# Kernel optimization log

Measured on AMD Instinct MI355X. Metric: run time of the kernel, lower is better.

## Reference

```python
import jax, jax.numpy as jnp
import numpy as np

E = 2048
H = 16
D = E // H  # head_dim = 128
S_SLOTS = 8
EPS = 1e-5


def _linear_params(key, fan_in, fan_out):
    kw, kb = jax.random.split(key)
    lim = 1.0 / np.sqrt(fan_in)
    W = jax.random.uniform(kw, (fan_out, fan_in), jnp.float32, -lim, lim)
    b = jax.random.uniform(kb, (fan_out,), jnp.float32, -lim, lim)
    return W, b


def setup_inputs() -> dict:
    key = jax.random.key(0)
    ks = jax.random.split(key, 10)
    x = jax.random.normal(ks[0], (2, 2048, E), jnp.float32)
    thought_slots = jax.random.normal(ks[1], (S_SLOTS, E), jnp.float32)
    Wq, bq = _linear_params(ks[2], E, E)
    Wk, bk = _linear_params(ks[3], E, E)
    Wv, bv = _linear_params(ks[4], E, E)
    Wtq, btq = _linear_params(ks[5], E, E)
    Wtk, btk = _linear_params(ks[6], E, E)
    Wtv, btv = _linear_params(ks[7], E, E)
    Wo, bo = _linear_params(ks[8], E, E)
    gamma = jnp.ones((E,), jnp.float32)
    beta = jnp.zeros((E,), jnp.float32)
    return dict(x=x, thought_slots=thought_slots, Wq=Wq, bq=bq, Wk=Wk, bk=bk,
                Wv=Wv, bv=bv, Wtq=Wtq, btq=btq, Wtk=Wtk, btk=btk,
                Wtv=Wtv, btv=btv, Wo=Wo, bo=bo, gamma=gamma, beta=beta)


def _heads(t, B):
    # [B, S, E] -> [B, H, S, D]
    return t.reshape(B, -1, H, D).transpose(0, 2, 1, 3)


def reference(x, thought_slots, Wq, bq, Wk, bk, Wv, bv,
              Wtq, btq, Wtk, btk, Wtv, btv, Wo, bo, gamma, beta):
    B, S, _ = x.shape
    scale = 1.0 / np.sqrt(D)

    # regular self-attention stream
    q = _heads(x @ Wq.T + bq, B)
    k = _heads(x @ Wk.T + bk, B)
    v = _heads(x @ Wv.T + bv, B)
    attn = jax.nn.softmax(jnp.einsum('bhqd,bhkd->bhqk', q, k) * scale, axis=-1)
    regular_out = jnp.einsum('bhqk,bhkd->bhqd', attn, v)

    # thought cross-attention stream (keys/values from learned slots)
    slots = jnp.broadcast_to(thought_slots, (B, S_SLOTS, thought_slots.shape[-1]))
    t_q = _heads(x @ Wtq.T + btq, B)
    t_k = _heads(slots @ Wtk.T + btk, B)
    t_v = _heads(slots @ Wtv.T + btv, B)
    t_attn = jax.nn.softmax(jnp.einsum('bhqd,bhkd->bhqk', t_q, t_k) * scale, axis=-1)
    thought_out = jnp.einsum('bhqk,bhkd->bhqd', t_attn, t_v)

    # merge heads, combine, layernorm, output projection
    combined = (regular_out + thought_out).transpose(0, 2, 1, 3).reshape(B, S, E)
    mu = jnp.mean(combined, axis=-1, keepdims=True)
    var = jnp.var(combined, axis=-1, keepdims=True)
    normed = (combined - mu) * jax.lax.rsqrt(var + EPS) * gamma + beta
    return normed @ Wo.T + bo
```

## Files before the change

kernel.cpp:

```cpp
#include <hip/hip_runtime.h>
#include <hip/hip_bf16.h>
#include <stdint.h>

typedef __bf16 bf16;
typedef __bf16 bf16x8 __attribute__((ext_vector_type(8)));
typedef __bf16 bf16x4 __attribute__((ext_vector_type(4)));
typedef float f32x4 __attribute__((ext_vector_type(4)));

#define E_DIM 2048
#define HEADS 16
#define HD 128
#define SEQ 2048
#define BATCH 2
#define NTOK 4096
#define NSLOT 8

#define QSCALE (0.08838834764831845f * 1.4426950408889634f)

__device__ __forceinline__ void gload_lds16(const void* g, void* lds) {
  __builtin_amdgcn_global_load_lds(
      (const __attribute__((address_space(1))) uint32_t*)g,
      (__attribute__((address_space(3))) uint32_t*)lds, 16, 0, 0);
}

__global__ __launch_bounds__(256) void cvt_f32_bf16_kernel(
    const float* __restrict__ src, bf16* __restrict__ dst, int n8)
{
  for (int i = blockIdx.x * 256 + threadIdx.x; i < n8; i += gridDim.x * 256) {
    const f32x4 a = *(const f32x4*)(src + i * 8);
    const f32x4 b = *(const f32x4*)(src + i * 8 + 4);
    bf16x8 o;
#pragma unroll
    for (int j = 0; j < 4; j++) { o[j] = (bf16)a[j]; o[4 + j] = (bf16)b[j]; }
    *(bf16x8*)(dst + i * 8) = o;
  }
}

struct ProjArgs {
  const bf16* W[4];
  const float* bias[4];
  void* out[4];
  int mode[4];
  float scale[4];
};

__global__ __launch_bounds__(512, 2) void gemm256_kernel(
    const bf16* __restrict__ A, ProjArgs pa, int nbm, int nbn)
{
  __shared__ bf16 As[2][256 * 64];
  __shared__ bf16 Bs[2][256 * 64];

  const int nwg = gridDim.x;
  const int qch = nwg >> 3;
  const int wg = (blockIdx.x & 7) * qch + (blockIdx.x >> 3);
  const int bm = wg % nbm;
  const int rest = wg / nbm;
  const int bn = rest % nbn;
  const int z = rest / nbn;

  const bf16* __restrict__ W = pa.W[z];
  const float* __restrict__ bias = pa.bias[z];
  void* __restrict__ out = pa.out[z];
  const int mode = pa.mode[z];
  const float scale = pa.scale[z];

  const int tid = threadIdx.x;
  const int lane = tid & 63;
  const int w = tid >> 6;
  const int wr = w >> 2;
  const int wc = w & 3;
  const int g = lane >> 4, c = lane & 15;

  const int rsub = lane >> 3;
  const int csub = ((lane & 7) ^ rsub) * 8;

  const int arow0 = wr * 128 + wc * 32;
  const int hb = wc >> 1, gj = (wr << 1) | (wc & 1);
  const int brow0 = hb * 128 + gj * 32;
  const bf16* Asrc = A + (size_t)(bm * 256 + arow0 + rsub) * 2048 + csub;
  const bf16* Bsrc = W + (size_t)(bn * 256 + brow0 + rsub) * 2048 + csub;

  auto stage = [&](int t, int buf) {
    const int k0 = t * 64;
    char* Adst = (char*)(&As[buf][0]) + arow0 * 128;
    char* Bdst = (char*)(&Bs[buf][0]) + brow0 * 128;
#pragma unroll
    for (int i = 0; i < 4; i++) {
      gload_lds16(Asrc + (size_t)(i * 8) * 2048 + k0, Adst + i * 1024);
      gload_lds16(Bsrc + (size_t)(i * 8) * 2048 + k0, Bdst + i * 1024);
    }
  };

  f32x4 acc[8][4] = {};

  stage(0, 0);
  __syncthreads();
  int cur = 0;

  const int NT = 2048 / 64;
  for (int t = 0; t < NT; t++) {
    if (t + 1 < NT) stage(t + 1, cur ^ 1);
#pragma unroll
    for (int kk = 0; kk < 2; kk++) {
      bf16x8 bfr[4], af[8];
#pragma unroll
      for (int n = 0; n < 4; n++) {
        const int row = wc * 64 + n * 16 + c;
        bfr[n] = *(const bf16x8*)((const char*)(&Bs[cur][0]) + row * 128 +
                                  (((kk * 4 + g) ^ (c & 7)) * 16));
      }
#pragma unroll
      for (int mi = 0; mi < 8; mi++) {
        const int row = wr * 128 + mi * 16 + c;
        af[mi] = *(const bf16x8*)((const char*)(&As[cur][0]) + row * 128 +
                                  (((kk * 4 + g) ^ (c & 7)) * 16));
      }
      __builtin_amdgcn_s_setprio(1);
#pragma unroll
      for (int mi = 0; mi < 8; mi++)
#pragma unroll
        for (int n = 0; n < 4; n++)
          acc[mi][n] = __builtin_amdgcn_mfma_f32_16x16x32_bf16(af[mi], bfr[n], acc[mi][n], 0, 0, 0);
      __builtin_amdgcn_s_setprio(0);
    }
    __syncthreads();
    cur ^= 1;
  }

#pragma unroll
  for (int mi = 0; mi < 8; mi++) {
#pragma unroll
    for (int n = 0; n < 4; n++) {
      const int col = bn * 256 + wc * 64 + n * 16 + c;
      const float bv = bias[col];
#pragma unroll
      for (int j = 0; j < 4; j++) {
        const int row = bm * 256 + wr * 128 + mi * 16 + g * 4 + j;
        const float v = (acc[mi][n][j] + bv) * scale;
        if (mode == 0) {
          ((float*)out)[(size_t)row * E_DIM + col] = v;
        } else {
          const int b = row >> 11, s = row & 2047;
          const int h = col >> 7, d = col & 127;
          size_t idx;
          if (mode == 1) idx = (((size_t)(b * HEADS + h)) * SEQ + s) * HD + d;
          else           idx = (((size_t)(b * HEADS + h)) * HD + d) * SEQ + s;
          ((bf16*)out)[idx] = (bf16)v;
        }
      }
    }
  }
}

__global__ __launch_bounds__(256) void gemm_nt_kernel(
    const bf16* __restrict__ A, ProjArgs pa, int M, int N, int K)
{
  __shared__ bf16 As[2][128 * 32];
  __shared__ bf16 Bs[2][128 * 32];

  const int z = blockIdx.z;
  const bf16* __restrict__ W = pa.W[z];
  const float* __restrict__ bias = pa.bias[z];
  void* __restrict__ out = pa.out[z];
  const int mode = pa.mode[z];
  const float scale = pa.scale[z];

  const int tid = threadIdx.x;
  const int lane = tid & 63;
  const int w = tid >> 6;
  const int wr = w >> 1, wc = w & 1;
  const int g = lane >> 4, c = lane & 15;
  const int bm = blockIdx.x, bn = blockIdx.y;

  f32x4 acc[4][4] = {};

  const int srow = lane >> 2;
  const int scol = (lane & 3) * 8;
  const bf16* Ab = A + (size_t)(bm * 128 + srow) * K + scol;
  const bf16* Wb = W + (size_t)(bn * 128 + srow) * K + scol;

  auto stage = [&](int k0, int buf) {
#pragma unroll
    for (int i = 0; i < 2; ++i) {
      const int chunk = w * 2 + i;
      gload_lds16(Ab + (size_t)(chunk * 16) * K + k0, (char*)(&As[buf][0]) + chunk * 1024);
      gload_lds16(Wb + (size_t)(chunk * 16) * K + k0, (char*)(&Bs[buf][0]) + chunk * 1024);
    }
  };

  stage(0, 0);
  __syncthreads();
  int cur = 0;

  for (int k0 = 0; k0 < K; k0 += 32) {
    if (k0 + 32 < K) stage(k0 + 32, cur ^ 1);
    bf16x8 af[4], bfr[4];
#pragma unroll
    for (int m = 0; m < 4; m++)
      af[m] = *(const bf16x8*)(&As[cur][0] + (wr * 64 + m * 16 + c) * 32 + g * 8);
#pragma unroll
    for (int n = 0; n < 4; n++)
      bfr[n] = *(const bf16x8*)(&Bs[cur][0] + (wc * 64 + n * 16 + c) * 32 + g * 8);
#pragma unroll
    for (int m = 0; m < 4; m++)
#pragma unroll
      for (int n = 0; n < 4; n++)
        acc[m][n] = __builtin_amdgcn_mfma_f32_16x16x32_bf16(af[m], bfr[n], acc[m][n], 0, 0, 0);
    __syncthreads();
    cur ^= 1;
  }

#pragma unroll
  for (int m = 0; m < 4; m++) {
#pragma unroll
    for (int n = 0; n < 4; n++) {
      const int col = bn * 128 + wc * 64 + n * 16 + c;
      const float bv = bias[col];
#pragma unroll
      for (int j = 0; j < 4; j++) {
        const int row = bm * 128 + wr * 64 + m * 16 + g * 4 + j;
        const float v = (acc[m][n][j] + bv) * scale;
        if (mode == 0) {
          ((float*)out)[(size_t)row * N + col] = v;
        } else {
          const int b = row >> 11, s = row & 2047;
          const int h = col >> 7, d = col & 127;
          size_t idx;
          if (mode == 1) idx = (((size_t)(b * HEADS + h)) * SEQ + s) * HD + d;
          else           idx = (((size_t)(b * HEADS + h)) * HD + d) * SEQ + s;
          ((bf16*)out)[idx] = (bf16)v;
        }
      }
    }
  }
}

__global__ __launch_bounds__(256) void slots_proj_kernel(
    const float* __restrict__ slots,
    const float* __restrict__ Wk, const float* __restrict__ bk,
    const float* __restrict__ Wv, const float* __restrict__ bv,
    float* __restrict__ tk, float* __restrict__ tv)
{
  const int col = blockIdx.x * 256 + threadIdx.x;
  const int slot = blockIdx.y;
  const int mat = blockIdx.z;
  const float* W = mat ? Wv : Wk;
  const float* bias = mat ? bv : bk;
  float* out = mat ? tv : tk;
  const float* xr = slots + (size_t)slot * E_DIM;
  const float* wr = W + (size_t)col * E_DIM;
  float acc = 0.f;
  for (int k = 0; k < E_DIM; k += 4) {
    const f32x4 a = *(const f32x4*)(xr + k);
    const f32x4 b4 = *(const f32x4*)(wr + k);
#pragma unroll
    for (int i = 0; i < 4; i++) acc += a[i] * b4[i];
  }
  out[(size_t)slot * E_DIM + col] = acc + bias[col];
}

__global__ __launch_bounds__(256) void flash_attn_kernel(
    const bf16* __restrict__ Qg, const bf16* __restrict__ Kg,
    const bf16* __restrict__ Vtg, bf16* __restrict__ Og)
{
  __shared__ char Ks[2][64 * 256];
  __shared__ char Vs[2][128 * 128];
  __shared__ char Ps[4][4096];

  const int orig = blockIdx.x;
  const int logical = (orig & 7) * 64 + (orig >> 3);
  const int qt = logical & 15;
  const int bh = logical >> 4;

  const int tid = threadIdx.x;
  const int lane = tid & 63;
  const int w = tid >> 6;
  const int g = lane >> 4, c = lane & 15;
  const int b = bh >> 4, h = bh & 15;
  const int q0 = qt * 128 + w * 32;

  const bf16* Qb = Qg + ((size_t)bh * SEQ + q0) * HD;
  const bf16* Kb = Kg + (size_t)bh * SEQ * HD;
  const bf16* Vb = Vtg + (size_t)bh * HD * SEQ;
  char* Pw = Ps[w];

  auto stage = [&](int kv0, int buf) {
#pragma unroll
    for (int i = 0; i < 4; i++) {
      const int chunk = w * 4 + i;
      const int p = chunk * 1024 + lane * 16;
      {
        const int r = p >> 8;
        const int sl = ((p >> 4) & 15) ^ (r & 7);
        gload_lds16(Kb + (size_t)(kv0 + r) * HD + sl * 8, &Ks[buf][0] + chunk * 1024);
      }
      {
        const int r = p >> 7;
        const int sl = ((p >> 4) & 7) ^ (r & 7);
        gload_lds16(Vb + (size_t)r * SEQ + kv0 + sl * 8, &Vs[buf][0] + chunk * 1024);
      }
    }
  };

  bf16x8 qf[4][2];
#pragma unroll
  for (int kk = 0; kk < 4; kk++)
#pragma unroll
    for (int n = 0; n < 2; n++)
      qf[kk][n] = *(const bf16x8*)(Qb + (size_t)(n * 16 + c) * HD + kk * 32 + g * 8);

  stage(0, 0);
  __syncthreads();
  int cur = 0;

  f32x4 acc[2][8] = {};
  float mrun[2] = {-1e30f, -1e30f};
  float lsum[2] = {0.f, 0.f};

  for (int kv0 = 0; kv0 < SEQ; kv0 += 64) {
    if (kv0 + 64 < SEQ) stage(kv0 + 64, cur ^ 1);

    f32x4 st[4][2] = {};
#pragma unroll
    for (int kk = 0; kk < 4; kk++) {
      bf16x8 kf[4];
#pragma unroll
      for (int kfr = 0; kfr < 4; kfr++) {
        const int r = kfr * 16 + c;
        const int sl = (kk * 4 + g) ^ (r & 7);
        kf[kfr] = *(const bf16x8*)(&Ks[cur][0] + r * 256 + sl * 16);
      }
      __builtin_amdgcn_s_setprio(1);
#pragma unroll
      for (int kfr = 0; kfr < 4; kfr++)
#pragma unroll
        for (int n = 0; n < 2; n++)
          st[kfr][n] = __builtin_amdgcn_mfma_f32_16x16x32_bf16(kf[kfr], qf[kk][n], st[kfr][n], 0, 0, 0);
      __builtin_amdgcn_s_setprio(0);
    }

    float fsc[2];
    bool anyresc = false;
#pragma unroll
    for (int n = 0; n < 2; n++) {
      float mt[8];
#pragma unroll
      for (int kfr = 0; kfr < 4; kfr++) {
        mt[kfr * 2]     = fmaxf(st[kfr][n][0], st[kfr][n][1]);
        mt[kfr * 2 + 1] = fmaxf(st[kfr][n][2], st[kfr][n][3]);
      }
#pragma unroll
      for (int i = 0; i < 4; i++) mt[i] = fmaxf(mt[i], mt[i + 4]);
      mt[0] = fmaxf(mt[0], mt[2]); mt[1] = fmaxf(mt[1], mt[3]);
      float lm = fmaxf(mt[0], mt[1]);
      lm = fmaxf(lm, __shfl_xor(lm, 16));
      lm = fmaxf(lm, __shfl_xor(lm, 32));
      if (__any(lm > mrun[n] + 8.0f)) {
        const float mn = fmaxf(mrun[n], lm);
        fsc[n] = exp2f(mrun[n] - mn);
        mrun[n] = mn;
        anyresc = true;
      } else {
        fsc[n] = 1.0f;
      }
      float stt[8];
#pragma unroll
      for (int kfr = 0; kfr < 4; kfr++) {
        float p0 = exp2f(st[kfr][n][0] - mrun[n]);
        float p1 = exp2f(st[kfr][n][1] - mrun[n]);
        float p2 = exp2f(st[kfr][n][2] - mrun[n]);
        float p3 = exp2f(st[kfr][n][3] - mrun[n]);
        st[kfr][n][0] = p0; st[kfr][n][1] = p1; st[kfr][n][2] = p2; st[kfr][n][3] = p3;
        stt[kfr * 2] = p0 + p1; stt[kfr * 2 + 1] = p2 + p3;
      }
#pragma unroll
      for (int i = 0; i < 4; i++) stt[i] += stt[i + 4];
      stt[0] += stt[2]; stt[1] += stt[3];
      lsum[n] = lsum[n] * fsc[n] + (stt[0] + stt[1]);
    }

    if (anyresc) {
#pragma unroll
      for (int m = 0; m < 2; m++)
#pragma unroll
        for (int j = 0; j < 4; j++) {
          const float fj = __shfl(fsc[m], (lane & 48) | (g * 4 + j));
#pragma unroll
          for (int n = 0; n < 8; n++) acc[m][n][j] *= fj;
        }
    }

#pragma unroll
    for (int n = 0; n < 2; n++)
#pragma unroll
      for (int kfr = 0; kfr < 4; kfr++) {
        bf16x4 pk;
#pragma unroll
        for (int j = 0; j < 4; j++) pk[j] = (bf16)st[kfr][n][j];
        const int q = n * 16 + c;
        const int L = q * 128 + kfr * 32 + g * 8;
        *(bf16x4*)(Pw + (L ^ ((q & 7) << 4))) = pk;
      }

#pragma unroll
    for (int kk = 0; kk < 2; kk++) {
      bf16x8 pf[2];
#pragma unroll
      for (int m = 0; m < 2; m++) {
        const int q = m * 16 + c;
        const int L = q * 128 + kk * 64 + g * 16;
        pf[m] = *(const bf16x8*)(Pw + (L ^ ((q & 7) << 4)));
      }
      __builtin_amdgcn_s_setprio(1);
#pragma unroll
      for (int n = 0; n < 8; n++) {
        const int d = n * 16 + c;
        const int Lv = d * 128 + kk * 64 + g * 16;
        const bf16x8 vf = *(const bf16x8*)(&Vs[cur][0] + (Lv ^ ((d & 7) << 4)));
#pragma unroll
        for (int m = 0; m < 2; m++)
          acc[m][n] = __builtin_amdgcn_mfma_f32_16x16x32_bf16(pf[m], vf, acc[m][n], 0, 0, 0);
      }
      __builtin_amdgcn_s_setprio(0);
    }

    __syncthreads();
    cur ^= 1;
  }

  float lrun[2];
#pragma unroll
  for (int n = 0; n < 2; n++) {
    float t = lsum[n];
    t += __shfl_xor(t, 16);
    t += __shfl_xor(t, 32);
    lrun[n] = t;
  }
#pragma unroll
  for (int m = 0; m < 2; m++) {
#pragma unroll
    for (int j = 0; j < 4; j++) {
      const float lb = __shfl(lrun[m], (lane & 48) | (g * 4 + j));
      const float linv = 1.0f / lb;
      const int s = q0 + m * 16 + g * 4 + j;
#pragma unroll
      for (int n = 0; n < 8; n++) {
        const int e = h * HD + n * 16 + c;
        Og[((size_t)b * SEQ + s) * E_DIM + e] = (bf16)(acc[m][n][j] * linv);
      }
    }
  }
}

__global__ __launch_bounds__(256) void thought_ln_kernel(
    const bf16* __restrict__ TQ, const float* __restrict__ TK,
    const float* __restrict__ TV, const bf16* __restrict__ ATT,
    const float* __restrict__ gamma, const float* __restrict__ beta,
    bf16* __restrict__ Y)
{
  __shared__ float wsum[4], wsq[4];
  const int tid = threadIdx.x;
  const int lane = tid & 63;
  const int w = tid >> 6;
  const int tok = blockIdx.x;
  const int b = tok >> 11, s = tok & 2047;
  const int e0 = tid * 8;
  const int h = e0 >> 7;
  const int d0 = e0 & 127;

  const bf16x8 av = *(const bf16x8*)(ATT + (size_t)tok * E_DIM + e0);
  float v[8];
#pragma unroll
  for (int i = 0; i < 8; i++) v[i] = (float)av[i];

  const bf16x8 qv8 = *(const bf16x8*)(TQ + (((size_t)(b * HEADS + h)) * SEQ + s) * HD + d0);
  float qv[8];
#pragma unroll
  for (int i = 0; i < 8; i++) qv[i] = (float)qv8[i];

  float dts[NSLOT];
#pragma unroll
  for (int sl = 0; sl < NSLOT; sl++) {
    const float* tkr = TK + (size_t)sl * E_DIM + e0;
    const f32x4 k0 = *(const f32x4*)(tkr);
    const f32x4 k1 = *(const f32x4*)(tkr + 4);
    float dp = 0.f;
#pragma unroll
    for (int i = 0; i < 4; i++) dp += qv[i] * k0[i] + qv[4 + i] * k1[i];
    dp += __shfl_xor(dp, 1);
    dp += __shfl_xor(dp, 2);
    dp += __shfl_xor(dp, 4);
    dp += __shfl_xor(dp, 8);
    dts[sl] = dp;
  }
  float mx = dts[0];
#pragma unroll
  for (int sl = 1; sl < NSLOT; sl++) mx = fmaxf(mx, dts[sl]);
  float p[NSLOT], den = 0.f;
#pragma unroll
  for (int sl = 0; sl < NSLOT; sl++) { p[sl] = exp2f(dts[sl] - mx); den += p[sl]; }
  const float dinv = 1.0f / den;
#pragma unroll
  for (int sl = 0; sl < NSLOT; sl++) {
    const float pn = p[sl] * dinv;
    const float* tvr = TV + (size_t)sl * E_DIM + e0;
    const f32x4 v0 = *(const f32x4*)(tvr);
    const f32x4 v1 = *(const f32x4*)(tvr + 4);
#pragma unroll
    for (int i = 0; i < 4; i++) { v[i] += pn * v0[i]; v[4 + i] += pn * v1[i]; }
  }

  float sm = 0.f, sq = 0.f;
#pragma unroll
  for (int i = 0; i < 8; i++) { sm += v[i]; sq += v[i] * v[i]; }
#pragma unroll
  for (int d = 1; d < 64; d <<= 1) { sm += __shfl_xor(sm, d); sq += __shfl_xor(sq, d); }
  if (lane == 0) { wsum[w] = sm; wsq[w] = sq; }
  __syncthreads();
  const float ts = wsum[0] + wsum[1] + wsum[2] + wsum[3];
  const float tq2 = wsq[0] + wsq[1] + wsq[2] + wsq[3];
  const float mean = ts * (1.f / E_DIM);
  const float var = tq2 * (1.f / E_DIM) - mean * mean;
  const float rstd = rsqrtf(var + 1e-5f);
  const f32x4 g0 = *(const f32x4*)(gamma + e0);
  const f32x4 g1 = *(const f32x4*)(gamma + e0 + 4);
  const f32x4 b0 = *(const f32x4*)(beta + e0);
  const f32x4 b1 = *(const f32x4*)(beta + e0 + 4);
  bf16x8 outv;
#pragma unroll
  for (int i = 0; i < 4; i++) {
    outv[i]     = (bf16)((v[i]     - mean) * rstd * g0[i] + b0[i]);
    outv[4 + i] = (bf16)((v[4 + i] - mean) * rstd * g1[i] + b1[i]);
  }
  *(bf16x8*)(Y + (size_t)tok * E_DIM + e0) = outv;
}

extern "C" void kernel_launch(void* const* d_in, const int* in_sizes, int n_in,
                              void* d_out, int out_size, void* d_ws, size_t ws_size,
                              hipStream_t stream) {
  (void)in_sizes; (void)n_in; (void)out_size; (void)ws_size;
  const float* x     = (const float*)d_in[0];
  const float* slots = (const float*)d_in[1];
  const float* Wq  = (const float*)d_in[2];   const float* bq  = (const float*)d_in[3];
  const float* Wk  = (const float*)d_in[4];   const float* bk  = (const float*)d_in[5];
  const float* Wv  = (const float*)d_in[6];   const float* bv  = (const float*)d_in[7];
  const float* Wtq = (const float*)d_in[8];   const float* btq = (const float*)d_in[9];
  const float* Wtk = (const float*)d_in[10];  const float* btk = (const float*)d_in[11];
  const float* Wtv = (const float*)d_in[12];  const float* btv = (const float*)d_in[13];
  const float* Wo  = (const float*)d_in[14];  const float* bo  = (const float*)d_in[15];
  const float* gamma = (const float*)d_in[16];
  const float* beta  = (const float*)d_in[17];

  uint8_t* ws = (uint8_t*)d_ws;
  const size_t BUF  = (size_t)NTOK * E_DIM * sizeof(bf16);
  const size_t WBUF = (size_t)E_DIM * E_DIM * sizeof(bf16);
  bf16* xb   = (bf16*)(ws + 0 * BUF);
  bf16* qb   = (bf16*)(ws + 1 * BUF);
  bf16* kb   = (bf16*)(ws + 2 * BUF);
  bf16* vtb  = (bf16*)(ws + 3 * BUF);
  bf16* tqb  = (bf16*)(ws + 4 * BUF);
  bf16* attb = (bf16*)(ws + 5 * BUF);
  bf16* nrmb = qb;
  uint8_t* wp = ws + 6 * BUF;
  bf16* Wqb  = (bf16*)(wp + 0 * WBUF);
  bf16* Wkb  = (bf16*)(wp + 1 * WBUF);
  bf16* Wvb  = (bf16*)(wp + 2 * WBUF);
  bf16* Wtqb = (bf16*)(wp + 3 * WBUF);
  bf16* Wob  = (bf16*)(wp + 4 * WBUF);
  float* tkb = (float*)(wp + 5 * WBUF);
  float* tvb = (float*)(wp + 5 * WBUF + 128 * 1024);

  const int WN8 = E_DIM * E_DIM / 8;
  const int XN8 = NTOK * E_DIM / 8;
  cvt_f32_bf16_kernel<<<dim3(2048), 256, 0, stream>>>(x, xb, XN8);
  cvt_f32_bf16_kernel<<<dim3(1024), 256, 0, stream>>>(Wq, Wqb, WN8);
  cvt_f32_bf16_kernel<<<dim3(1024), 256, 0, stream>>>(Wk, Wkb, WN8);
  cvt_f32_bf16_kernel<<<dim3(1024), 256, 0, stream>>>(Wv, Wvb, WN8);
  cvt_f32_bf16_kernel<<<dim3(1024), 256, 0, stream>>>(Wtq, Wtqb, WN8);
  cvt_f32_bf16_kernel<<<dim3(1024), 256, 0, stream>>>(Wo, Wob, WN8);

  ProjArgs pa;
  pa.W[0] = Wqb;  pa.bias[0] = bq;  pa.out[0] = qb;  pa.mode[0] = 1; pa.scale[0] = QSCALE;
  pa.W[1] = Wkb;  pa.bias[1] = bk;  pa.out[1] = kb;  pa.mode[1] = 1; pa.scale[1] = 1.0f;
  pa.W[2] = Wvb;  pa.bias[2] = bv;  pa.out[2] = vtb; pa.mode[2] = 2; pa.scale[2] = 1.0f;
  pa.W[3] = Wtqb; pa.bias[3] = btq; pa.out[3] = tqb; pa.mode[3] = 1; pa.scale[3] = QSCALE;
  gemm256_kernel<<<dim3(16 * 8 * 4), 512, 0, stream>>>(xb, pa, 16, 8);

  slots_proj_kernel<<<dim3(E_DIM / 256, NSLOT, 2), 256, 0, stream>>>(
      slots, Wtk, btk, Wtv, btv, tkb, tvb);

  flash_attn_kernel<<<dim3((SEQ / 128) * BATCH * HEADS), 256, 0, stream>>>(
      qb, kb, vtb, attb);
  thought_ln_kernel<<<dim3(NTOK), 256, 0, stream>>>(
      tqb, tkb, tvb, attb, gamma, beta, nrmb);

  ProjArgs po;
  po.W[0] = Wob; po.bias[0] = bo; po.out[0] = d_out; po.mode[0] = 0; po.scale[0] = 1.0f;
  po.W[1] = po.W[2] = po.W[3] = Wob;
  po.bias[1] = po.bias[2] = po.bias[3] = bo;
  po.out[1] = po.out[2] = po.out[3] = d_out;
  po.mode[1] = po.mode[2] = po.mode[3] = 0;
  po.scale[1] = po.scale[2] = po.scale[3] = 1.0f;
  gemm_nt_kernel<<<dim3(NTOK / 128, E_DIM / 128, 1), 256, 0, stream>>>(
      nrmb, po, NTOK, E_DIM, E_DIM);
}
```

Measured before the change: 523.9 us.

## Rewrite flash attention with 32x32 MFMA, register-resident P, 512-thread blocks

The flash attention kernel switches from 16x16x32 to 32x32x16 bf16 MFMA tiles, so each wave owns 32 query rows with a single running max and sum per lane. The P matrix is now rearranged in registers with a cross-half lane shuffle instead of a per-wave LDS round trip, which removes the Ps shared buffer and its write/read traffic. Blocks grow to 512 threads covering 256 queries, so each staged K/V tile is shared by eight waves, and the K swizzle widens to 16. The cost is higher register pressure from the f32x16 accumulators and half as many blocks in the grid, which may lower occupancy.

```diff
diff --git a/kernel.cpp b/kernel.cpp
--- a/kernel.cpp
+++ b/kernel.cpp
@@ -6,6 +6,9 @@
 typedef __bf16 bf16x8 __attribute__((ext_vector_type(8)));
 typedef __bf16 bf16x4 __attribute__((ext_vector_type(4)));
 typedef float f32x4 __attribute__((ext_vector_type(4)));
+typedef float f32x16 __attribute__((ext_vector_type(16)));
+typedef uint32_t u32x2 __attribute__((ext_vector_type(2)));
+typedef uint32_t u32x4 __attribute__((ext_vector_type(4)));
 
 #define E_DIM 2048
 #define HEADS 16
@@ -259,197 +262,161 @@
   out[(size_t)slot * E_DIM + col] = acc + bias[col];
 }
 
-__global__ __launch_bounds__(256) void flash_attn_kernel(
+__global__ __launch_bounds__(512) void flash_attn_kernel(
     const bf16* __restrict__ Qg, const bf16* __restrict__ Kg,
     const bf16* __restrict__ Vtg, bf16* __restrict__ Og)
 {
   __shared__ char Ks[2][64 * 256];
   __shared__ char Vs[2][128 * 128];
-  __shared__ char Ps[4][4096];
 
   const int orig = blockIdx.x;
-  const int logical = (orig & 7) * 64 + (orig >> 3);
-  const int qt = logical & 15;
-  const int bh = logical >> 4;
+  const int logical = (orig & 7) * 32 + (orig >> 3);
+  const int qt = logical & 7;
+  const int bh = logical >> 3;
 
   const int tid = threadIdx.x;
   const int lane = tid & 63;
   const int w = tid >> 6;
-  const int g = lane >> 4, c = lane & 15;
+  const int q = lane & 31;
+  const int hi = lane >> 5;
   const int b = bh >> 4, h = bh & 15;
-  const int q0 = qt * 128 + w * 32;
+  const int q0 = qt * 256 + w * 32;
 
   const bf16* Qb = Qg + ((size_t)bh * SEQ + q0) * HD;
   const bf16* Kb = Kg + (size_t)bh * SEQ * HD;
   const bf16* Vb = Vtg + (size_t)bh * HD * SEQ;
-  char* Pw = Ps[w];
 
   auto stage = [&](int kv0, int buf) {
 #pragma unroll
-    for (int i = 0; i < 4; i++) {
-      const int chunk = w * 4 + i;
-      const int p = chunk * 1024 + lane * 16;
-      {
-        const int r = p >> 8;
-        const int sl = ((p >> 4) & 15) ^ (r & 7);
-        gload_lds16(Kb + (size_t)(kv0 + r) * HD + sl * 8, &Ks[buf][0] + chunk * 1024);
-      }
-      {
-        const int r = p >> 7;
-        const int sl = ((p >> 4) & 7) ^ (r & 7);
-        gload_lds16(Vb + (size_t)r * SEQ + kv0 + sl * 8, &Vs[buf][0] + chunk * 1024);
-      }
+    for (int i = 0; i < 2; i++) {
+      const int p = (tid + i * 512) * 16;
+      { const int r = p >> 8; const int s16 = (p >> 4) & 15;
+        gload_lds16(Kb + (size_t)(kv0 + r) * HD + (s16 ^ (r & 15)) * 8, &Ks[buf][0] + p); }
+      { const int r = p >> 7; const int s8 = (p >> 4) & 7;
+        gload_lds16(Vb + (size_t)r * SEQ + kv0 + (s8 ^ (r & 7)) * 8, &Vs[buf][0] + p); }
     }
   };
 
-  bf16x8 qf[4][2];
-#pragma unroll
-  for (int kk = 0; kk < 4; kk++)
-#pragma unroll
-    for (int n = 0; n < 2; n++)
-      qf[kk][n] = *(const bf16x8*)(Qb + (size_t)(n * 16 + c) * HD + kk * 32 + g * 8);
+  bf16x8 qf[8];
+#pragma unroll
+  for (int kc = 0; kc < 8; kc++)
+    qf[kc] = *(const bf16x8*)(Qb + (size_t)q * HD + kc * 16 + hi * 8);
 
   stage(0, 0);
   __syncthreads();
   int cur = 0;
 
-  f32x4 acc[2][8] = {};
-  float mrun[2] = {-1e30f, -1e30f};
-  float lsum[2] = {0.f, 0.f};
+  f32x16 o[4] = {};
+  float mrun = -1e30f, lsum = 0.f;
 
   for (int kv0 = 0; kv0 < SEQ; kv0 += 64) {
     if (kv0 + 64 < SEQ) stage(kv0 + 64, cur ^ 1);
 
-    f32x4 st[4][2] = {};
-#pragma unroll
-    for (int kk = 0; kk < 4; kk++) {
-      bf16x8 kf[4];
-#pragma unroll
-      for (int kfr = 0; kfr < 4; kfr++) {
-        const int r = kfr * 16 + c;
-        const int sl = (kk * 4 + g) ^ (r & 7);
-        kf[kfr] = *(const bf16x8*)(&Ks[cur][0] + r * 256 + sl * 16);
-      }
-      __builtin_amdgcn_s_setprio(1);
-#pragma unroll
-      for (int kfr = 0; kfr < 4; kfr++)
-#pragma unroll
-        for (int n = 0; n < 2; n++)
-          st[kfr][n] = __builtin_amdgcn_mfma_f32_16x16x32_bf16(kf[kfr], qf[kk][n], st[kfr][n], 0, 0, 0);
-      __builtin_amdgcn_s_setprio(0);
-    }
-
-    float fsc[2];
-    bool anyresc = false;
-#pragma unroll
-    for (int n = 0; n < 2; n++) {
-      float mt[8];
-#pragma unroll
-      for (int kfr = 0; kfr < 4; kfr++) {
-        mt[kfr * 2]     = fmaxf(st[kfr][n][0], st[kfr][n][1]);
-        mt[kfr * 2 + 1] = fmaxf(st[kfr][n][2], st[kfr][n][3]);
-      }
-#pragma unroll
-      for (int i = 0; i < 4; i++) mt[i] = fmaxf(mt[i], mt[i + 4]);
-      mt[0] = fmaxf(mt[0], mt[2]); mt[1] = fmaxf(mt[1], mt[3]);
-      float lm = fmaxf(mt[0], mt[1]);
-      lm = fmaxf(lm, __shfl_xor(lm, 16));
-      lm = fmaxf(lm, __shfl_xor(lm, 32));
-      if (__any(lm > mrun[n] + 8.0f)) {
-        const float mn = fmaxf(mrun[n], lm);
-        fsc[n] = exp2f(mrun[n] - mn);
-        mrun[n] = mn;
-        anyresc = true;
-      } else {
-        fsc[n] = 1.0f;
-      }
-      float stt[8];
-#pragma unroll
-      for (int kfr = 0; kfr < 4; kfr++) {
-        float p0 = exp2f(st[kfr][n][0] - mrun[n]);
-        float p1 = exp2f(st[kfr][n][1] - mrun[n]);
-        float p2 = exp2f(st[kfr][n][2] - mrun[n]);
-        float p3 = exp2f(st[kfr][n][3] - mrun[n]);
-        st[kfr][n][0] = p0; st[kfr][n][1] = p1; st[kfr][n][2] = p2; st[kfr][n][3] = p3;
-        stt[kfr * 2] = p0 + p1; stt[kfr * 2 + 1] = p2 + p3;
-      }
-#pragma unroll
-      for (int i = 0; i < 4; i++) stt[i] += stt[i + 4];
-      stt[0] += stt[2]; stt[1] += stt[3];
-      lsum[n] = lsum[n] * fsc[n] + (stt[0] + stt[1]);
-    }
-
-    if (anyresc) {
-#pragma unroll
-      for (int m = 0; m < 2; m++)
-#pragma unroll
-        for (int j = 0; j < 4; j++) {
-          const float fj = __shfl(fsc[m], (lane & 48) | (g * 4 + j));
-#pragma unroll
-          for (int n = 0; n < 8; n++) acc[m][n][j] *= fj;
+    f32x16 st[2] = {};
+    __builtin_amdgcn_s_setprio(1);
+#pragma unroll
+    for (int kc = 0; kc < 8; kc++) {
+#pragma unroll
+      for (int blk = 0; blk < 2; blk++) {
+        const int rt = blk * 32 + q;
+        const int sl = (2 * kc + hi) ^ (rt & 15);
+        const bf16x8 kf = *(const bf16x8*)(&Ks[cur][0] + rt * 256 + sl * 16);
+        st[blk] = __builtin_amdgcn_mfma_f32_32x32x16_bf16(kf, qf[kc], st[blk], 0, 0, 0);
+      }
+    }
+    __builtin_amdgcn_s_setprio(0);
+
+    float t[16];
+#pragma unroll
+    for (int i = 0; i < 16; i++) t[i] = fmaxf(st[0][i], st[1][i]);
+#pragma unroll
+    for (int s2 = 8; s2 > 0; s2 >>= 1)
+#pragma unroll
+      for (int i = 0; i < 8; i++) if (i < s2) t[i] = fmaxf(t[i], t[i + s2]);
+    float lm = t[0];
+    lm = fmaxf(lm, __shfl_xor(lm, 32));
+
+    float fsc = 1.0f;
+    if (__any(lm > mrun + 8.0f)) {
+      const float mn = fmaxf(mrun, lm);
+      fsc = exp2f(mrun - mn);
+      mrun = mn;
+#pragma unroll
+      for (int db = 0; db < 4; db++)
+#pragma unroll
+        for (int i = 0; i < 16; i++) o[db][i] *= fsc;
+    }
+
+    float ps0 = 0.f, ps1 = 0.f, ps2 = 0.f, ps3 = 0.f;
+#pragma unroll
+    for (int blk = 0; blk < 2; blk++)
+#pragma unroll
+      for (int i = 0; i < 16; i += 4) {
+        const float p0 = exp2f(st[blk][i]     - mrun);
+        const float p1 = exp2f(st[blk][i + 1] - mrun);
+        const float p2 = exp2f(st[blk][i + 2] - mrun);
+        const float p3 = exp2f(st[blk][i + 3] - mrun);
+        st[blk][i] = p0; st[blk][i + 1] = p1; st[blk][i + 2] = p2; st[blk][i + 3] = p3;
+        ps0 += p0; ps1 += p1; ps2 += p2; ps3 += p3;
+      }
+    lsum = lsum * fsc + ((ps0 + ps1) + (ps2 + ps3));
+
+    bf16x8 pb[2][2];
+#pragma unroll
+    for (int blk = 0; blk < 2; blk++)
+#pragma unroll
+      for (int c = 0; c < 2; c++) {
+        bf16x4 Lv, Hv;
+#pragma unroll
+        for (int i = 0; i < 4; i++) {
+          Lv[i] = (bf16)st[blk][8 * c + i];
+          Hv[i] = (bf16)st[blk][8 * c + 4 + i];
         }
-    }
-
-#pragma unroll
-    for (int n = 0; n < 2; n++)
-#pragma unroll
-      for (int kfr = 0; kfr < 4; kfr++) {
-        bf16x4 pk;
-#pragma unroll
-        for (int j = 0; j < 4; j++) pk[j] = (bf16)st[kfr][n][j];
-        const int q = n * 16 + c;
-        const int L = q * 128 + kfr * 32 + g * 8;
-        *(bf16x4*)(Pw + (L ^ ((q & 7) << 4))) = pk;
-      }
-
-#pragma unroll
-    for (int kk = 0; kk < 2; kk++) {
-      bf16x8 pf[2];
-#pragma unroll
-      for (int m = 0; m < 2; m++) {
-        const int q = m * 16 + c;
-        const int L = q * 128 + kk * 64 + g * 16;
-        pf[m] = *(const bf16x8*)(Pw + (L ^ ((q & 7) << 4)));
-      }
-      __builtin_amdgcn_s_setprio(1);
-#pragma unroll
-      for (int n = 0; n < 8; n++) {
-        const int d = n * 16 + c;
-        const int Lv = d * 128 + kk * 64 + g * 16;
-        const bf16x8 vf = *(const bf16x8*)(&Vs[cur][0] + (Lv ^ ((d & 7) << 4)));
-#pragma unroll
-        for (int m = 0; m < 2; m++)
-          acc[m][n] = __builtin_amdgcn_mfma_f32_16x16x32_bf16(pf[m], vf, acc[m][n], 0, 0, 0);
-      }
-      __builtin_amdgcn_s_setprio(0);
-    }
+        const u32x2 Lu = __builtin_bit_cast(u32x2, Lv);
+        const u32x2 Hu = __builtin_bit_cast(u32x2, Hv);
+        const uint32_t s0 = hi ? Lu.x : Hu.x;
+        const uint32_t s1 = hi ? Lu.y : Hu.y;
+        const uint32_t x0 = (uint32_t)__shfl_xor((int)s0, 32);
+        const uint32_t x1 = (uint32_t)__shfl_xor((int)s1, 32);
+        u32x4 bv;
+        bv.x = hi ? x0 : Lu.x;
+        bv.y = hi ? x1 : Lu.y;
+        bv.z = hi ? Hu.x : x0;
+        bv.w = hi ? Hu.y : x1;
+        pb[blk][c] = __builtin_bit_cast(bf16x8, bv);
+      }
+
+    __builtin_amdgcn_s_setprio(1);
+#pragma unroll
+    for (int db = 0; db < 4; db++) {
+      const int rt = db * 32 + q;
+#pragma unroll
+      for (int blk = 0; blk < 2; blk++)
+#pragma unroll
+        for (int c = 0; c < 2; c++) {
+          const int sl = (blk * 4 + c * 2 + hi) ^ (rt & 7);
+          const bf16x8 vf = *(const bf16x8*)(&Vs[cur][0] + rt * 128 + sl * 16);
+          o[db] = __builtin_amdgcn_mfma_f32_32x32x16_bf16(vf, pb[blk][c], o[db], 0, 0, 0);
+        }
+    }
+    __builtin_amdgcn_s_setprio(0);
 
     __syncthreads();
     cur ^= 1;
   }
 
-  float lrun[2];
-#pragma unroll
-  for (int n = 0; n < 2; n++) {
-    float t = lsum[n];
-    t += __shfl_xor(t, 16);
-    t += __shfl_xor(t, 32);
-    lrun[n] = t;
-  }
-#pragma unroll
-  for (int m = 0; m < 2; m++) {
-#pragma unroll
-    for (int j = 0; j < 4; j++) {
-      const float lb = __shfl(lrun[m], (lane & 48) | (g * 4 + j));
-      const float linv = 1.0f / lb;
-      const int s = q0 + m * 16 + g * 4 + j;
-#pragma unroll
-      for (int n = 0; n < 8; n++) {
-        const int e = h * HD + n * 16 + c;
-        Og[((size_t)b * SEQ + s) * E_DIM + e] = (bf16)(acc[m][n][j] * linv);
-      }
-    }
-  }
+  const float lt = lsum + __shfl_xor(lsum, 32);
+  const float linv = 1.0f / lt;
+  bf16* Orow = Og + ((size_t)b * SEQ + q0 + q) * E_DIM + h * HD;
+#pragma unroll
+  for (int db = 0; db < 4; db++)
+#pragma unroll
+    for (int g4 = 0; g4 < 4; g4++) {
+      bf16x4 ov;
+#pragma unroll
+      for (int i = 0; i < 4; i++) ov[i] = (bf16)(o[db][g4 * 4 + i] * linv);
+      *(bf16x4*)(Orow + db * 32 + g4 * 8 + hi * 4) = ov;
+    }
 }
 
 __global__ __launch_bounds__(256) void thought_ln_kernel(
@@ -589,7 +556,7 @@
   slots_proj_kernel<<<dim3(E_DIM / 256, NSLOT, 2), 256, 0, stream>>>(
       slots, Wtk, btk, Wtv, btv, tkb, tvb);
 
-  flash_attn_kernel<<<dim3((SEQ / 128) * BATCH * HEADS), 256, 0, stream>>>(
+  flash_attn_kernel<<<dim3((SEQ / 256) * BATCH * HEADS), 512, 0, stream>>>(
       qb, kb, vtb, attb);
   thought_ln_kernel<<<dim3(NTOK), 256, 0, stream>>>(
       tqb, tkb, tvb, attb, gamma, beta, nrmb);
```

Result: faster. 455.8 us (-13.0%).
